# Kernel tuning notes

Measured on AMD Instinct MI355X. Metric: run time of the kernel, lower is better.

Reference implementation:

```python
import jax, jax.numpy as jnp
import numpy as np

NUM_EMB = 1024
EMB_DIM = 32


def setup_inputs() -> dict:
    key = jax.random.key(0)
    k1, k2 = jax.random.split(key)
    z = jax.random.normal(k1, (32, EMB_DIM, 64, 64), dtype=jnp.float32)
    # nn.Embedding weight init: uniform(-1/num_embeddings, 1/num_embeddings)
    emb_weight = jax.random.uniform(
        k2, (NUM_EMB, EMB_DIM), dtype=jnp.float32,
        minval=-1.0 / NUM_EMB, maxval=1.0 / NUM_EMB)
    return {"z": z, "emb_weight": emb_weight}


def reference(z, emb_weight):
    # z: [B, C, H, W] -> [B, H, W, C]
    z_p = jnp.transpose(z, (0, 2, 3, 1))
    B, H, W, C = z_p.shape
    z_flat = z_p.reshape(-1, C)  # [N, C]
    # squared distances via expansion: ||z||^2 + ||e||^2 - 2 z.e  -> [N, K]
    d = (jnp.sum(z_flat * z_flat, axis=1, keepdims=True)
         + jnp.sum(emb_weight * emb_weight, axis=1)
         - 2.0 * jnp.matmul(z_flat, emb_weight.T))
    idx = jnp.argmin(d, axis=1)  # [N]
    z_q = emb_weight[idx].reshape(B, H, W, C)
    # straight-through estimator (applied in BHWC, then back to BCHW)
    z_q = z_p + jax.lax.stop_gradient(z_q - z_p)
    z_q = jnp.transpose(z_q, (0, 3, 1, 2))  # [B, C, H, W]
    return z_q, idx
```

## Files before the change

kernel.cpp:

```cpp
#include <hip/hip_runtime.h>


#define NUM_EMB 1024
#define EMB_DIM 32
#define HW      4096
#define BATCH   32
#define N_TOT   (BATCH * HW)
#define NSPLIT  4
#define CODES_PER (NUM_EMB / NSPLIT)
#define MARGIN  1.0e-4f
#define CHUNK   256
#define ESTRIDE 36
#define OVF_CAP 131072

#define OFF_BQ   0u
#define OFF_EH   4096u
#define OFF_EL   69632u
#define OFF_CNT  135168u
#define OFF_CAND 659456u
#define OFF_OVFC 4853760u
#define OFF_OVFL 4853776u
#define WS_NEED  5378064u
#define WS_NEED_R7 (4096u + 4u * 131072u * 8u)

using bf16x8 = __attribute__((ext_vector_type(8))) short;
using bf16x4 = __attribute__((ext_vector_type(4))) short;
using f32x4  = __attribute__((ext_vector_type(4))) float;

#define REPEAT32(M) \
    M(0)  M(1)  M(2)  M(3)  M(4)  M(5)  M(6)  M(7)  \
    M(8)  M(9)  M(10) M(11) M(12) M(13) M(14) M(15) \
    M(16) M(17) M(18) M(19) M(20) M(21) M(22) M(23) \
    M(24) M(25) M(26) M(27) M(28) M(29) M(30) M(31)

__device__ __forceinline__ unsigned short bf16_rne(float x) {
    unsigned u = __float_as_uint(x);
    return (unsigned short)((u + 0x7FFFu + ((u >> 16) & 1u)) >> 16);
}

__device__ __forceinline__ float pairwise_sq32(const float* __restrict__ e) {
    float r0 = __fmul_rn(e[0], e[0]), r1 = __fmul_rn(e[1], e[1]);
    float r2 = __fmul_rn(e[2], e[2]), r3 = __fmul_rn(e[3], e[3]);
    float r4 = __fmul_rn(e[4], e[4]), r5 = __fmul_rn(e[5], e[5]);
    float r6 = __fmul_rn(e[6], e[6]), r7 = __fmul_rn(e[7], e[7]);
#pragma unroll
    for (int i = 8; i < 32; i += 8) {
        r0 = __fadd_rn(r0, __fmul_rn(e[i + 0], e[i + 0]));
        r1 = __fadd_rn(r1, __fmul_rn(e[i + 1], e[i + 1]));
        r2 = __fadd_rn(r2, __fmul_rn(e[i + 2], e[i + 2]));
        r3 = __fadd_rn(r3, __fmul_rn(e[i + 3], e[i + 3]));
        r4 = __fadd_rn(r4, __fmul_rn(e[i + 4], e[i + 4]));
        r5 = __fadd_rn(r5, __fmul_rn(e[i + 5], e[i + 5]));
        r6 = __fadd_rn(r6, __fmul_rn(e[i + 6], e[i + 6]));
        r7 = __fadd_rn(r7, __fmul_rn(e[i + 7], e[i + 7]));
    }
    return __fadd_rn(__fadd_rn(__fadd_rn(r0, r1), __fadd_rn(r2, r3)),
                     __fadd_rn(__fadd_rn(r4, r5), __fadd_rn(r6, r7)));
}

__device__ __forceinline__ void store_row16(unsigned short* dst,
                                            const unsigned short* v) {
    unsigned w[16];
#pragma unroll
    for (int i = 0; i < 16; ++i)
        w[i] = (unsigned)v[2 * i] | ((unsigned)v[2 * i + 1] << 16);
    uint4* d4 = (uint4*)dst;
    d4[0] = make_uint4(w[0], w[1], w[2], w[3]);
    d4[1] = make_uint4(w[4], w[5], w[6], w[7]);
    d4[2] = make_uint4(w[8], w[9], w[10], w[11]);
    d4[3] = make_uint4(w[12], w[13], w[14], w[15]);
}

__global__ __launch_bounds__(256) void vq_prep_e(
        const float* __restrict__ emb, float* __restrict__ bq,
        unsigned short* __restrict__ eh, unsigned short* __restrict__ el,
        int* __restrict__ ovfc) {
    const int j = blockIdx.x * 256 + threadIdx.x;
    if (j == 0) *ovfc = 0;
    if (j >= NUM_EMB) return;
    const float* e = emb + j * EMB_DIM;
    bq[j] = pairwise_sq32(e);
    unsigned short h[32], l[32];
#pragma unroll
    for (int c = 0; c < 32; ++c) {
        float v = e[c];
        unsigned short hb = bf16_rne(v);
        float hf = __uint_as_float((unsigned)hb << 16);
        l[c] = bf16_rne(v - hf);
        h[c] = hb;
    }
    store_row16(eh + (size_t)j * 32, h);
    store_row16(el + (size_t)j * 32, l);
}

__device__ __forceinline__ bf16x8 lds_read8(const short* p) {
    bf16x4 a = *(const bf16x4*)p;
    bf16x4 b = *(const bf16x4*)(p + 4);
    return __builtin_shufflevector(a, b, 0, 1, 2, 3, 4, 5, 6, 7);
}

__global__ __launch_bounds__(256, 4) void vq_filter(
        const float* __restrict__ z,
        const unsigned short* __restrict__ eh,
        const unsigned short* __restrict__ el,
        const float* __restrict__ bq, int* __restrict__ cnt,
        int* __restrict__ cand) {
    __shared__ __align__(16) short seh[CHUNK * ESTRIDE];
    __shared__ __align__(16) short sel[CHUNK * ESTRIDE];
    __shared__ float sbq[CHUNK];

    const int tid  = threadIdx.x;
    const int lane = tid & 63;
    const int wv   = tid >> 6;
    const int cloc = lane & 15, quad = lane >> 4;
    const int qbase = blockIdx.x * 128 + wv * 32;

    bf16x8 azh[2], azl[2];
#pragma unroll
    for (int t = 0; t < 2; ++t) {
        const int q  = qbase + t * 16 + cloc;
        const int b  = q >> 12;
        const int hw = q & 4095;
        const float* zb = z + ((size_t)b * EMB_DIM + quad * 8) * HW + hw;
#pragma unroll
        for (int k = 0; k < 8; ++k) {
            float v = zb[(size_t)k * HW];
            unsigned short hb = bf16_rne(v);
            float hf = __uint_as_float((unsigned)hb << 16);
            azh[t][k] = (short)hb;
            azl[t][k] = (short)bf16_rne(v - hf);
        }
    }

    float m1[2][4], m2[2][4], m3[2][4];
    int   i1[2][4], i2[2][4];
#pragma unroll
    for (int t = 0; t < 2; ++t)
#pragma unroll
        for (int r = 0; r < 4; ++r) {
            m1[t][r] = 3.4e38f; m2[t][r] = 3.4e38f; m3[t][r] = 3.4e38f;
            i1[t][r] = 0;       i2[t][r] = 0;
        }

    for (int ch = 0; ch < 4; ++ch) {
        if (ch) __syncthreads();
#pragma unroll
        for (int i = 0; i < 8; ++i) {
            const int chunk = i * 256 + tid;
            const int r = chunk >> 3, c = chunk & 7;
            *(uint2*)&seh[r * ESTRIDE + c * 4] =
                *(const uint2*)(eh + (size_t)(ch * CHUNK + r) * 32 + c * 4);
            *(uint2*)&sel[r * ESTRIDE + c * 4] =
                *(const uint2*)(el + (size_t)(ch * CHUNK + r) * 32 + c * 4);
        }
        sbq[tid] = bq[ch * CHUNK + tid];
        __syncthreads();

        for (int jt = 0; jt < 16; ++jt) {
            const int row = jt * 16 + cloc;
            bf16x8 efh = lds_read8(&seh[row * ESTRIDE + quad * 8]);
            bf16x8 efl = lds_read8(&sel[row * ESTRIDE + quad * 8]);
            const float bqv = sbq[row];
            const int jts = ch * 16 + jt;
#pragma unroll
            for (int t = 0; t < 2; ++t) {
                f32x4 acc = {0.f, 0.f, 0.f, 0.f};
                acc = __builtin_amdgcn_mfma_f32_16x16x32_bf16(azl[t], efh, acc, 0, 0, 0);
                acc = __builtin_amdgcn_mfma_f32_16x16x32_bf16(azh[t], efl, acc, 0, 0, 0);
                acc = __builtin_amdgcn_mfma_f32_16x16x32_bf16(azh[t], efh, acc, 0, 0, 0);
#pragma unroll
                for (int r = 0; r < 4; ++r) {
                    const float tt = __fmaf_rn(-2.0f, acc[r], bqv);
                    const bool l1 = tt < m1[t][r];
                    const bool l2 = tt < m2[t][r];
                    const bool l3 = tt < m3[t][r];
                    m3[t][r] = l2 ? m2[t][r] : (l3 ? tt : m3[t][r]);
                    m2[t][r] = l1 ? m1[t][r] : (l2 ? tt : m2[t][r]);
                    i2[t][r] = l1 ? i1[t][r] : (l2 ? jts : i2[t][r]);
                    m1[t][r] = l1 ? tt  : m1[t][r];
                    i1[t][r] = l1 ? jts : i1[t][r];
                }
            }
        }
    }

    float g[2][4];
#pragma unroll
    for (int t = 0; t < 2; ++t)
#pragma unroll
        for (int r = 0; r < 4; ++r) g[t][r] = m1[t][r];
#pragma unroll
    for (int off = 1; off < 16; off <<= 1)
#pragma unroll
        for (int t = 0; t < 2; ++t)
#pragma unroll
            for (int r = 0; r < 4; ++r)
                g[t][r] = fminf(g[t][r], __shfl_xor(g[t][r], off, 64));

#pragma unroll
    for (int t = 0; t < 2; ++t)
#pragma unroll
        for (int r = 0; r < 4; ++r) {
            const float thr = g[t][r] + MARGIN;
            const int q = qbase + t * 16 + quad * 4 + r;
            if (m1[t][r] <= thr) {
                int pos = atomicAdd(&cnt[q], 1);
                if (pos < 8) cand[(q << 3) + pos] = i1[t][r] * 16 + cloc;
            }
            if (m2[t][r] <= thr) {
                int pos = atomicAdd(&cnt[q], 1);
                if (pos < 8) cand[(q << 3) + pos] = i2[t][r] * 16 + cloc;
            }
            if (m3[t][r] <= thr) atomicAdd(&cnt[q], 1000);
        }
}

#define LOADZ(c) float z##c = zp[(size_t)(c) * HW];
#define Z_SQ_A()                                                              \
    float r0 = __fmul_rn(z0, z0), r1 = __fmul_rn(z1, z1);                     \
    float r2 = __fmul_rn(z2, z2), r3 = __fmul_rn(z3, z3);                     \
    float r4 = __fmul_rn(z4, z4), r5 = __fmul_rn(z5, z5);                     \
    float r6 = __fmul_rn(z6, z6), r7 = __fmul_rn(z7, z7);                     \
    r0 = __fadd_rn(r0, __fmul_rn(z8,  z8));  r0 = __fadd_rn(r0, __fmul_rn(z16, z16)); \
    r0 = __fadd_rn(r0, __fmul_rn(z24, z24));                                  \
    r1 = __fadd_rn(r1, __fmul_rn(z9,  z9));  r1 = __fadd_rn(r1, __fmul_rn(z17, z17)); \
    r1 = __fadd_rn(r1, __fmul_rn(z25, z25));                                  \
    r2 = __fadd_rn(r2, __fmul_rn(z10, z10)); r2 = __fadd_rn(r2, __fmul_rn(z18, z18)); \
    r2 = __fadd_rn(r2, __fmul_rn(z26, z26));                                  \
    r3 = __fadd_rn(r3, __fmul_rn(z11, z11)); r3 = __fadd_rn(r3, __fmul_rn(z19, z19)); \
    r3 = __fadd_rn(r3, __fmul_rn(z27, z27));                                  \
    r4 = __fadd_rn(r4, __fmul_rn(z12, z12)); r4 = __fadd_rn(r4, __fmul_rn(z20, z20)); \
    r4 = __fadd_rn(r4, __fmul_rn(z28, z28));                                  \
    r5 = __fadd_rn(r5, __fmul_rn(z13, z13)); r5 = __fadd_rn(r5, __fmul_rn(z21, z21)); \
    r5 = __fadd_rn(r5, __fmul_rn(z29, z29));                                  \
    r6 = __fadd_rn(r6, __fmul_rn(z14, z14)); r6 = __fadd_rn(r6, __fmul_rn(z22, z22)); \
    r6 = __fadd_rn(r6, __fmul_rn(z30, z30));                                  \
    r7 = __fadd_rn(r7, __fmul_rn(z15, z15)); r7 = __fadd_rn(r7, __fmul_rn(z23, z23)); \
    r7 = __fadd_rn(r7, __fmul_rn(z31, z31));                                  \
    const float a = __fadd_rn(                                                \
        __fadd_rn(__fadd_rn(r0, r1), __fadd_rn(r2, r3)),                      \
        __fadd_rn(__fadd_rn(r4, r5), __fadd_rn(r6, r7)));

#define FMA1(k) m = __fmaf_rn(z##k, e[(k)], m);
#define EXACT_KEY(jv)                                                         \
    {                                                                         \
        const float* e = emb + (size_t)(jv) * EMB_DIM;                        \
        float m = 0.0f;                                                       \
        REPEAT32(FMA1)                                                        \
        float d = __fsub_rn(__fadd_rn(a, bq[(jv)]), __fmul_rn(2.0f, m));      \
        unsigned u = __float_as_uint(d);                                      \
        u = (u & 0x80000000u) ? ~u : (u | 0x80000000u);                       \
        unsigned long long kk =                                               \
            ((unsigned long long)u << 32) | (unsigned)(jv);                   \
        if (kk < bestk) bestk = kk;                                           \
    }

__global__ __launch_bounds__(256, 2) void vq_pass3(
        const float* __restrict__ z, const float* __restrict__ emb,
        const float* __restrict__ bq, const int* __restrict__ cnt,
        const int* __restrict__ cand, int* __restrict__ ovfc,
        int* __restrict__ ovfl, float* __restrict__ out_zq,
        float* __restrict__ out_idx) {
    const int n  = blockIdx.x * 256 + threadIdx.x;
    const int b  = n >> 12;
    const int hw = n & 4095;
    const int c = cnt[n];
    if (c < 1 || c > 8) {
        int pos = atomicAdd(ovfc, 1);
        if (pos < OVF_CAP) { ovfl[pos] = n; return; }
    }
    const float* zp = z + (size_t)b * EMB_DIM * HW + hw;
    REPEAT32(LOADZ)
    Z_SQ_A()

    unsigned long long bestk = ~0ull;
    if (c >= 1 && c <= 8) {
        for (int i = 0; i < c; ++i) { const int jv = cand[(n << 3) + i]; EXACT_KEY(jv) }
    } else {
        for (int jv = 0; jv < NUM_EMB; ++jv) EXACT_KEY(jv)
    }
    const int bidx = (int)(unsigned)(bestk & 0xffffffffu);
    out_idx[n] = (float)bidx;
    const float* eb = emb + (size_t)bidx * EMB_DIM;
    float* op = out_zq + (size_t)b * EMB_DIM * HW + hw;
#pragma unroll
    for (int cc = 0; cc < EMB_DIM; ++cc) op[(size_t)cc * HW] = eb[cc];
}

__global__ __launch_bounds__(256) void vq_fixup(
        const float* __restrict__ z, const float* __restrict__ emb,
        const float* __restrict__ bq, const int* __restrict__ ovfc,
        const int* __restrict__ ovfl, float* __restrict__ out_zq,
        float* __restrict__ out_idx) {
    __shared__ unsigned long long bs[256];
    const int tid = threadIdx.x;
    int total = *ovfc;
    if (total > OVF_CAP) total = OVF_CAP;

    for (int it = blockIdx.x; it < total; it += gridDim.x) {
        const int n  = ovfl[it];
        const int b  = n >> 12;
        const int hw = n & 4095;
        const float* zp = z + (size_t)b * EMB_DIM * HW + hw;
        REPEAT32(LOADZ)
        Z_SQ_A()
        unsigned long long bestk = ~0ull;
#pragma unroll
        for (int k = 0; k < 4; ++k) { const int jv = tid * 4 + k; EXACT_KEY(jv) }
        bs[tid] = bestk;
        __syncthreads();
        for (int off = 128; off > 0; off >>= 1) {
            if (tid < off && bs[tid + off] < bs[tid]) bs[tid] = bs[tid + off];
            __syncthreads();
        }
        const int bidx = (int)(unsigned)(bs[0] & 0xffffffffu);
        if (tid == 0) out_idx[n] = (float)bidx;
        if (tid < EMB_DIM)
            out_zq[(size_t)b * EMB_DIM * HW + (size_t)tid * HW + hw] =
                emb[(size_t)bidx * EMB_DIM + tid];
        __syncthreads();
    }
}

#define SCAN_GROUP4(j)                                                        \
    {                                                                         \
        const float* e = emb + (size_t)(j) * EMB_DIM;                         \
        const float bq0 = bq[(j) + 0], bq1 = bq[(j) + 1];                     \
        const float bq2 = bq[(j) + 2], bq3 = bq[(j) + 3];                     \
        float m0 = 0.0f, m1 = 0.0f, m2 = 0.0f, m3 = 0.0f;                     \
        REPEAT32(FMA_K)                                                       \
        float d0 = __fsub_rn(__fadd_rn(a, bq0), __fmul_rn(2.0f, m0));         \
        float d1 = __fsub_rn(__fadd_rn(a, bq1), __fmul_rn(2.0f, m1));         \
        float d2 = __fsub_rn(__fadd_rn(a, bq2), __fmul_rn(2.0f, m2));         \
        float d3 = __fsub_rn(__fadd_rn(a, bq3), __fmul_rn(2.0f, m3));         \
        if (d0 < best) { best = d0; bidx = (j) + 0; }                         \
        if (d1 < best) { best = d1; bidx = (j) + 1; }                         \
        if (d2 < best) { best = d2; bidx = (j) + 2; }                         \
        if (d3 < best) { best = d3; bidx = (j) + 3; }                         \
    }
#define FMA_K(k) \
        m0 = __fmaf_rn(z##k, e[0 * EMB_DIM + (k)], m0); \
        m1 = __fmaf_rn(z##k, e[1 * EMB_DIM + (k)], m1); \
        m2 = __fmaf_rn(z##k, e[2 * EMB_DIM + (k)], m2); \
        m3 = __fmaf_rn(z##k, e[3 * EMB_DIM + (k)], m3);

__global__ __launch_bounds__(256) void vq_sqnorm_kernel(
        const float* __restrict__ emb, float* __restrict__ bq) {
    int j = blockIdx.x * 256 + threadIdx.x;
    if (j < NUM_EMB) bq[j] = pairwise_sq32(emb + j * EMB_DIM);
}

__global__ __launch_bounds__(128, 4) void vq_partial_kernel(
        const float* __restrict__ z, const float* __restrict__ emb,
        const float* __restrict__ bq, unsigned long long* __restrict__ pk) {
    const int n  = blockIdx.x * 128 + threadIdx.x;
    const int b  = n >> 12;
    const int hw = n & 4095;
    const float* zp = z + (size_t)b * EMB_DIM * HW + hw;
    REPEAT32(LOADZ)
    Z_SQ_A()
    const int j0 = blockIdx.y * CODES_PER;
    float best = 3.4e38f;
    int   bidx = j0;
    for (int j = j0; j < j0 + CODES_PER; j += 4) SCAN_GROUP4(j)
    pk[(size_t)blockIdx.y * N_TOT + n] =
        ((unsigned long long)__float_as_uint(best) << 32) | (unsigned)bidx;
}

__global__ __launch_bounds__(256, 2) void vq_main_kernel(
        const float* __restrict__ z, const float* __restrict__ emb,
        const float* __restrict__ bq, float* __restrict__ out_zq,
        float* __restrict__ out_idx) {
    const int n  = blockIdx.x * 256 + threadIdx.x;
    const int b  = n >> 12;
    const int hw = n & 4095;
    const float* zp = z + (size_t)b * EMB_DIM * HW + hw;
    REPEAT32(LOADZ)
    Z_SQ_A()
    float best = 3.4e38f;
    int   bidx = 0;
    for (int j = 0; j < NUM_EMB; j += 4) SCAN_GROUP4(j)
    out_idx[n] = (float)bidx;
    const float* eb = emb + (size_t)bidx * EMB_DIM;
    float* op = out_zq + (size_t)b * EMB_DIM * HW + hw;
#pragma unroll
    for (int cc = 0; cc < EMB_DIM; ++cc) op[(size_t)cc * HW] = eb[cc];
}

__global__ __launch_bounds__(256) void vq_combine_kernel(
        const float* __restrict__ emb,
        const unsigned long long* __restrict__ pk,
        float* __restrict__ out_zq, float* __restrict__ out_idx) {
    const int n = blockIdx.x * 256 + threadIdx.x;
    unsigned long long m = pk[n];
#pragma unroll
    for (int y = 1; y < NSPLIT; ++y) {
        unsigned long long v = pk[(size_t)y * N_TOT + n];
        if (v < m) m = v;
    }
    const int bidx = (int)(unsigned)(m & 0xffffffffu);
    out_idx[n] = (float)bidx;
    const int b  = n >> 12;
    const int hw = n & 4095;
    const float* eb = emb + (size_t)bidx * EMB_DIM;
    float* op = out_zq + (size_t)b * EMB_DIM * HW + hw;
#pragma unroll
    for (int cc = 0; cc < EMB_DIM; ++cc) op[(size_t)cc * HW] = eb[cc];
}

extern "C" void kernel_launch(void* const* d_in, const int* in_sizes, int n_in,
                              void* d_out, int out_size, void* d_ws,
                              size_t ws_size, hipStream_t stream) {
    const float* z   = (const float*)d_in[0];
    const float* emb = (const float*)d_in[1];
    char* ws = (char*)d_ws;
    float* out0 = (float*)d_out;
    float* out1 = out0 + (size_t)BATCH * EMB_DIM * HW;

    if (ws_size >= WS_NEED) {
        float*          bq   = (float*)(ws + OFF_BQ);
        unsigned short* eh   = (unsigned short*)(ws + OFF_EH);
        unsigned short* el   = (unsigned short*)(ws + OFF_EL);
        int*            cnt  = (int*)(ws + OFF_CNT);
        int*            cand = (int*)(ws + OFF_CAND);
        int*            ovfc = (int*)(ws + OFF_OVFC);
        int*            ovfl = (int*)(ws + OFF_OVFL);

        hipMemsetAsync(cnt, 0, N_TOT * sizeof(int), stream);
        vq_prep_e<<<NUM_EMB / 256, 256, 0, stream>>>(emb, bq, eh, el, ovfc);
        vq_filter<<<N_TOT / 128, 256, 0, stream>>>(z, eh, el, bq, cnt, cand);
        vq_pass3<<<N_TOT / 256, 256, 0, stream>>>(z, emb, bq, cnt, cand,
                                                  ovfc, ovfl, out0, out1);
        vq_fixup<<<1024, 256, 0, stream>>>(z, emb, bq, ovfc, ovfl,
                                           out0, out1);
    } else if (ws_size >= WS_NEED_R7) {
        float* bq = (float*)ws;
        unsigned long long* pk = (unsigned long long*)(ws + 4096);
        vq_sqnorm_kernel<<<NUM_EMB / 256, 256, 0, stream>>>(emb, bq);
        vq_partial_kernel<<<dim3(N_TOT / 128, NSPLIT), 128, 0, stream>>>(
            z, emb, bq, pk);
        vq_combine_kernel<<<N_TOT / 256, 256, 0, stream>>>(emb, pk, out0, out1);
    } else {
        float* bq = (float*)ws;
        vq_sqnorm_kernel<<<NUM_EMB / 256, 256, 0, stream>>>(emb, bq);
        vq_main_kernel<<<N_TOT / 256, 256, 0, stream>>>(z, emb, bq, out0, out1);
    }
}
```

Measured before the change: 150.2 us.

## Fold -2 and norm into MFMA, track top-1 only, skip exact rescoring for single candidates

The embedding is pre-scaled by -2 and the accumulator is seeded with the code norm, which removes the per-element FMA after the MFMAs. The filter now keeps only the best and second-best distance per lane. It emits a single candidate and flags a near-tie on the runner-up to the overflow path, dropping the third-place tracking. Pass3 takes the lone candidate directly without reloading z or computing exact distances, and the counter memset is folded into the prep kernel launch. These trade more fallback-path work on ties and a capless overflow write for less register pressure and less per-query rescoring.

```diff
diff --git a/kernel.cpp b/kernel.cpp
--- a/kernel.cpp
+++ b/kernel.cpp
@@ -74,23 +74,24 @@
 __global__ __launch_bounds__(256) void vq_prep_e(
         const float* __restrict__ emb, float* __restrict__ bq,
         unsigned short* __restrict__ eh, unsigned short* __restrict__ el,
-        int* __restrict__ ovfc) {
-    const int j = blockIdx.x * 256 + threadIdx.x;
-    if (j == 0) *ovfc = 0;
-    if (j >= NUM_EMB) return;
-    const float* e = emb + j * EMB_DIM;
-    bq[j] = pairwise_sq32(e);
+        int* __restrict__ cnt, int* __restrict__ ovfc) {
+    const int g = blockIdx.x * 256 + threadIdx.x;
+    cnt[g] = 0;
+    if (g == 0) *ovfc = 0;
+    if (g >= NUM_EMB) return;
+    const float* e = emb + g * EMB_DIM;
+    bq[g] = pairwise_sq32(e);
     unsigned short h[32], l[32];
 #pragma unroll
     for (int c = 0; c < 32; ++c) {
-        float v = e[c];
+        float v = -2.0f * e[c];
         unsigned short hb = bf16_rne(v);
         float hf = __uint_as_float((unsigned)hb << 16);
         l[c] = bf16_rne(v - hf);
         h[c] = hb;
     }
-    store_row16(eh + (size_t)j * 32, h);
-    store_row16(el + (size_t)j * 32, l);
+    store_row16(eh + (size_t)g * 32, h);
+    store_row16(el + (size_t)g * 32, l);
 }
 
 __device__ __forceinline__ bf16x8 lds_read8(const short* p) {
@@ -132,14 +133,13 @@
         }
     }
 
-    float m1[2][4], m2[2][4], m3[2][4];
-    int   i1[2][4], i2[2][4];
+    float m1[2][4], m2[2][4];
+    int   i1[2][4];
 #pragma unroll
     for (int t = 0; t < 2; ++t)
 #pragma unroll
         for (int r = 0; r < 4; ++r) {
-            m1[t][r] = 3.4e38f; m2[t][r] = 3.4e38f; m3[t][r] = 3.4e38f;
-            i1[t][r] = 0;       i2[t][r] = 0;
+            m1[t][r] = 3.4e38f; m2[t][r] = 3.4e38f; i1[t][r] = 0;
         }
 
     for (int ch = 0; ch < 4; ++ch) {
@@ -164,19 +164,16 @@
             const int jts = ch * 16 + jt;
 #pragma unroll
             for (int t = 0; t < 2; ++t) {
-                f32x4 acc = {0.f, 0.f, 0.f, 0.f};
+                f32x4 acc = {bqv, bqv, bqv, bqv};
                 acc = __builtin_amdgcn_mfma_f32_16x16x32_bf16(azl[t], efh, acc, 0, 0, 0);
                 acc = __builtin_amdgcn_mfma_f32_16x16x32_bf16(azh[t], efl, acc, 0, 0, 0);
                 acc = __builtin_amdgcn_mfma_f32_16x16x32_bf16(azh[t], efh, acc, 0, 0, 0);
 #pragma unroll
                 for (int r = 0; r < 4; ++r) {
-                    const float tt = __fmaf_rn(-2.0f, acc[r], bqv);
+                    const float tt = acc[r];
                     const bool l1 = tt < m1[t][r];
                     const bool l2 = tt < m2[t][r];
-                    const bool l3 = tt < m3[t][r];
-                    m3[t][r] = l2 ? m2[t][r] : (l3 ? tt : m3[t][r]);
                     m2[t][r] = l1 ? m1[t][r] : (l2 ? tt : m2[t][r]);
-                    i2[t][r] = l1 ? i1[t][r] : (l2 ? jts : i2[t][r]);
                     m1[t][r] = l1 ? tt  : m1[t][r];
                     i1[t][r] = l1 ? jts : i1[t][r];
                 }
@@ -207,11 +204,7 @@
                 int pos = atomicAdd(&cnt[q], 1);
                 if (pos < 8) cand[(q << 3) + pos] = i1[t][r] * 16 + cloc;
             }
-            if (m2[t][r] <= thr) {
-                int pos = atomicAdd(&cnt[q], 1);
-                if (pos < 8) cand[(q << 3) + pos] = i2[t][r] * 16 + cloc;
-            }
-            if (m3[t][r] <= thr) atomicAdd(&cnt[q], 1000);
+            if (m2[t][r] <= thr) atomicAdd(&cnt[q], 1000);
         }
 }
 
@@ -267,19 +260,20 @@
     const int c = cnt[n];
     if (c < 1 || c > 8) {
         int pos = atomicAdd(ovfc, 1);
-        if (pos < OVF_CAP) { ovfl[pos] = n; return; }
-    }
-    const float* zp = z + (size_t)b * EMB_DIM * HW + hw;
-    REPEAT32(LOADZ)
-    Z_SQ_A()
-
-    unsigned long long bestk = ~0ull;
-    if (c >= 1 && c <= 8) {
+        ovfl[pos] = n;
+        return;
+    }
+    int bidx;
+    if (c == 1) {
+        bidx = cand[n << 3];
+    } else {
+        const float* zp = z + (size_t)b * EMB_DIM * HW + hw;
+        REPEAT32(LOADZ)
+        Z_SQ_A()
+        unsigned long long bestk = ~0ull;
         for (int i = 0; i < c; ++i) { const int jv = cand[(n << 3) + i]; EXACT_KEY(jv) }
-    } else {
-        for (int jv = 0; jv < NUM_EMB; ++jv) EXACT_KEY(jv)
-    }
-    const int bidx = (int)(unsigned)(bestk & 0xffffffffu);
+        bidx = (int)(unsigned)(bestk & 0xffffffffu);
+    }
     out_idx[n] = (float)bidx;
     const float* eb = emb + (size_t)bidx * EMB_DIM;
     float* op = out_zq + (size_t)b * EMB_DIM * HW + hw;
@@ -426,8 +420,7 @@
         int*            ovfc = (int*)(ws + OFF_OVFC);
         int*            ovfl = (int*)(ws + OFF_OVFL);
 
-        hipMemsetAsync(cnt, 0, N_TOT * sizeof(int), stream);
-        vq_prep_e<<<NUM_EMB / 256, 256, 0, stream>>>(emb, bq, eh, el, ovfc);
+        vq_prep_e<<<N_TOT / 256, 256, 0, stream>>>(emb, bq, eh, el, cnt, ovfc);
         vq_filter<<<N_TOT / 128, 256, 0, stream>>>(z, eh, el, bq, cnt, cand);
         vq_pass3<<<N_TOT / 256, 256, 0, stream>>>(z, emb, bq, cnt, cand,
                                                   ovfc, ovfl, out0, out1);
```

Result: faster. 140.5 us (-6.5%).
